# Performance work log

Measured on AMD Instinct MI355X. Metric: run time of the kernel, lower is better.

Reference implementation:

```python
import jax, jax.numpy as jnp
import numpy as np

N_HEADS = 16
HEAD_DIM = 64
ATTN_WINDOW = 128
ROPE_BASE = 10000.0


def _rotate_half(x):
    # (x0, x1) -> (-x1, x0) over interleaved pairs in the last dim
    xr = x.reshape(*x.shape[:-1], -1, 2)
    out = jnp.stack((-xr[..., 1], xr[..., 0]), axis=-1)
    return out.reshape(x.shape)


def _rope_cos_sin(T, rotary_dim, base, dtype):
    inv_freq = 1.0 / (base ** (jnp.arange(0, rotary_dim, 2, dtype=jnp.float32) / rotary_dim))
    t = jnp.arange(T, dtype=jnp.float32)
    freqs = t[:, None] * inv_freq[None, :]            # (T, rotary_dim/2)
    cos = jnp.repeat(jnp.cos(freqs), 2, axis=-1)      # (T, rotary_dim)
    sin = jnp.repeat(jnp.sin(freqs), 2, axis=-1)
    return cos.astype(dtype), sin.astype(dtype)


def _apply_rope(x, cos, sin):
    # x: (B, H, T, Dh); rotary_dim == Dh here (rope_fraction = 1.0)
    c = cos[None, None, :, :]
    s = sin[None, None, :, :]
    return x * c + _rotate_half(x) * s


def setup_inputs() -> dict:
    key = jax.random.key(0)
    ks = jax.random.split(key, 5)
    B, T, C = 2, 2048, 1024
    x = jax.random.normal(ks[0], (B, T, C), dtype=jnp.float32)
    Wqkv = jax.random.normal(ks[1], (C, 3 * C), dtype=jnp.float32) * 0.02
    bqkv = jax.random.normal(ks[2], (3 * C,), dtype=jnp.float32) * 0.02
    Wproj = jax.random.normal(ks[3], (C, C), dtype=jnp.float32) * 0.02
    bproj = jax.random.normal(ks[4], (C,), dtype=jnp.float32) * 0.02
    return {"x": x, "Wqkv": Wqkv, "bqkv": bqkv, "Wproj": Wproj, "bproj": bproj}


def reference(x, Wqkv, bqkv, Wproj, bproj):
    B, T, C = x.shape
    H, Dh = N_HEADS, HEAD_DIM

    qkv = x @ Wqkv + bqkv                              # (B, T, 3C)
    q, k, v = jnp.split(qkv, 3, axis=-1)

    def heads(t):
        return t.reshape(B, T, H, Dh).transpose(0, 2, 1, 3)  # (B, H, T, Dh)
    q, k, v = heads(q), heads(k), heads(v)

    cos, sin = _rope_cos_sin(T, Dh, ROPE_BASE, x.dtype)
    q = _apply_rope(q, cos, sin)
    k = _apply_rope(k, cos, sin)

    # local causal mask: allowed iff 0 <= i - j < attn_window
    idx = jnp.arange(T)
    rel = idx[:, None] - idx[None, :]
    allowed = (rel >= 0) & (rel < ATTN_WINDOW)         # (T, T)

    scale = 1.0 / jnp.sqrt(jnp.asarray(Dh, dtype=x.dtype))
    scores = jnp.einsum("bhqd,bhkd->bhqk", q, k) * scale
    scores = jnp.where(allowed[None, None], scores, jnp.asarray(-jnp.inf, dtype=x.dtype))
    attn = jax.nn.softmax(scores, axis=-1)
    attn_out = jnp.einsum("bhqk,bhkd->bhqd", attn, v)  # (B, H, T, Dh)

    attn_out = attn_out.transpose(0, 2, 1, 3).reshape(B, T, C)
    return attn_out @ Wproj + bproj
```

## Files before the change

### kernel.cpp

```cpp
#include <hip/hip_runtime.h>


using bf16x8 = short  __attribute__((ext_vector_type(8)));
using f32x4  = float __attribute__((ext_vector_type(4)));

__device__ __forceinline__ float bf2f(unsigned short u) {
    return __uint_as_float(((unsigned int)u) << 16);
}
__device__ __forceinline__ unsigned short f2bf(float f) {
    unsigned int u = __float_as_uint(f);
    u += 0x7fffu + ((u >> 16) & 1u);
    return (unsigned short)(u >> 16);
}

__device__ __forceinline__ void gload_lds16(const unsigned short* g,
                                            unsigned short* l) {
    __builtin_amdgcn_global_load_lds(
        (const __attribute__((address_space(1))) unsigned int*)(g),
        (__attribute__((address_space(3))) unsigned int*)(l),
        16, 0, 0);
}

template <int N>
__device__ __forceinline__ void vm_wait() {
    static_assert(N == 0 || N == 2 || N == 3 || N == 4 || N == 6, "add case");
    if constexpr (N == 0)      asm volatile("s_waitcnt vmcnt(0)" ::: "memory");
    else if constexpr (N == 2) asm volatile("s_waitcnt vmcnt(2)" ::: "memory");
    else if constexpr (N == 3) asm volatile("s_waitcnt vmcnt(3)" ::: "memory");
    else if constexpr (N == 4) asm volatile("s_waitcnt vmcnt(4)" ::: "memory");
    else                       asm volatile("s_waitcnt vmcnt(6)" ::: "memory");
}
__device__ __forceinline__ void lgkm_wait0() {
    asm volatile("s_waitcnt lgkmcnt(0)" ::: "memory");
}

__global__ __launch_bounds__(256) void prep_kernel(
        const float* __restrict__ Wqkv, const float* __restrict__ Wproj,
        const float* __restrict__ x,
        unsigned short* __restrict__ WqkvT, unsigned short* __restrict__ WprojT,
        unsigned short* __restrict__ xb, float* __restrict__ tab) {
    __shared__ unsigned short tile[32][33];
    int blk = blockIdx.x;
    int tid = threadIdx.x;
    if (blk < 4096) {
        const float* W; unsigned short* WT; int cols, bx, by;
        if (blk < 3072) { W = Wqkv;  WT = WqkvT;  cols = 3072; bx = blk % 96; by = blk / 96; }
        else            { W = Wproj; WT = WprojT; cols = 1024; bx = (blk - 3072) & 31; by = (blk - 3072) >> 5; }
        int c0 = bx * 32, r0 = by * 32;
        int tx = tid & 31, ty = tid >> 5;
        for (int i = ty; i < 32; i += 8)
            tile[i][tx] = f2bf(W[(size_t)(r0 + i) * cols + c0 + tx]);
        __syncthreads();
        for (int i = ty; i < 32; i += 8)
            WT[(size_t)(c0 + i) * 1024 + r0 + tx] = tile[tx][i];
    } else if (blk < 5120) {
        for (int i = (blk - 4096) * 256 + tid; i < 1048576; i += 262144) {
            float4 v = ((const float4*)x)[i];
            ushort4 o;
            o.x = f2bf(v.x); o.y = f2bf(v.y); o.z = f2bf(v.z); o.w = f2bf(v.w);
            ((ushort4*)xb)[i] = o;
        }
    } else {
        int idx = (blk - 5120) * 256 + tid;
        int t = idx >> 5, i = idx & 31;
        float inv = powf(10000.0f, -(float)i / 32.0f);
        float ang = (float)t * inv;
        tab[idx * 2]     = cosf(ang);
        tab[idx * 2 + 1] = sinf(ang);
    }
}

__global__ __launch_bounds__(256) void gemm1_adirect(
        const unsigned short* __restrict__ A,
        const unsigned short* __restrict__ Bt,
        const float* __restrict__ bias,
        unsigned short* __restrict__ C,
        const float* __restrict__ tab,
        int M, int N, int K) {
    __shared__ unsigned short smem[128 * 128];
    auto Bs = [&](int buf) { return &smem[buf * 128 * 32]; };

    int nwg = gridDim.x * gridDim.y;
    int lid = blockIdx.y * gridDim.x + blockIdx.x;
    int orig = (lid & 7) * (nwg >> 3) + (lid >> 3);
    int bx = orig % gridDim.x, by = orig / gridDim.x;
    int row0 = by * 128, col0 = bx * 128;

    int tid = threadIdx.x;
    int lane = tid & 63, wid = tid >> 6;
    int wr = wid >> 1, wc = wid & 1;
    int fr = lane & 15, kq = lane >> 4;
    int r_in = lane >> 2;
    int scg8 = (((lane & 3) ^ ((lane >> 3) & 3))) * 8;
    int kqs8 = (kq ^ ((fr >> 1) & 3)) * 8;

    f32x4 acc[4][4];
    #pragma unroll
    for (int i = 0; i < 4; ++i)
        #pragma unroll
        for (int j = 0; j < 4; ++j)
            acc[i][j] = (f32x4){0.f, 0.f, 0.f, 0.f};

    auto stageB = [&](int buf, int kt) {
        #pragma unroll
        for (int t = 0; t < 2; ++t) {
            int jb = wid * 2 + t;
            int row = jb * 16 + r_in;
            gload_lds16(Bt + (size_t)(col0 + row) * K + kt + scg8,
                        Bs(buf) + jb * 512);
        }
    };

    const unsigned short* Arow =
        A + (size_t)(row0 + wr * 64 + fr) * K + kq * 8;

    int nt = K >> 5;
    stageB(0, 0);
    for (int t = 0; t < nt; ++t) {
        int kt = t << 5;
        bf16x8 af[4];
        #pragma unroll
        for (int i = 0; i < 4; ++i)
            af[i] = *(const bf16x8*)(Arow + (size_t)(i * 16) * K + kt);
        __builtin_amdgcn_sched_barrier(0);
        if (t + 1 < nt) {
            stageB((t + 1) & 1, kt + 32);
            vm_wait<6>();
        } else {
            vm_wait<4>();
        }
        __builtin_amdgcn_s_barrier();
        bf16x8 bfv[4];
        #pragma unroll
        for (int j = 0; j < 4; ++j)
            bfv[j] = *(const bf16x8*)&Bs(t & 1)[(wc * 64 + j * 16 + fr) * 32 + kqs8];
        #pragma unroll
        for (int i = 0; i < 4; ++i)
            #pragma unroll
            for (int j = 0; j < 4; ++j)
                acc[i][j] = __builtin_amdgcn_mfma_f32_16x16x32_bf16(
                                af[i], bfv[j], acc[i][j], 0, 0, 0);
        if (t + 1 < nt) {
            lgkm_wait0();
            __builtin_amdgcn_s_barrier();
        }
    }

    int rg = kq * 4;
    unsigned short* Ct = smem;
    __syncthreads();
    #pragma unroll
    for (int j = 0; j < 4; ++j) {
        int colL = wc * 64 + j * 16 + fr;
        float bz = bias[col0 + colL];
        #pragma unroll
        for (int i = 0; i < 4; ++i) {
            float v4[4];
            #pragma unroll
            for (int r = 0; r < 4; ++r) v4[r] = acc[i][j][r] + bz;
            if (col0 < 2048) {
                int ii2 = (colL & 63) >> 1;
                bool odd = fr & 1;
                #pragma unroll
                for (int r = 0; r < 4; ++r) {
                    float part = __shfl_xor(v4[r], 1);
                    int trow = (row0 + wr * 64 + i * 16 + rg + r) & 2047;
                    float cc2 = tab[(trow * 32 + ii2) * 2];
                    float ss = tab[(trow * 32 + ii2) * 2 + 1];
                    v4[r] = odd ? fmaf(v4[r], cc2,  part * ss)
                                : fmaf(v4[r], cc2, -part * ss);
                }
            }
            #pragma unroll
            for (int r = 0; r < 4; ++r)
                Ct[(wr * 64 + i * 16 + rg + r) * 128 + colL] = f2bf(v4[r]);
        }
    }
    __syncthreads();
    #pragma unroll
    for (int p = 0; p < 8; ++p) {
        int idx = p * 256 + tid;
        int row = idx >> 4;
        int c8v = (idx & 15) * 8;
        *(bf16x8*)&C[(size_t)(row0 + row) * N + col0 + c8v] =
            *(const bf16x8*)&Ct[row * 128 + c8v];
    }
}

template <int BM, int BN, int WM, int WN, bool OUT_BF16, int DEPTH>
__global__ __launch_bounds__(256) void gemm_lds(
        const unsigned short* __restrict__ A,
        const unsigned short* __restrict__ Bt,
        const float* __restrict__ bias,
        void* __restrict__ Cv,
        int M, int N, int K) {
    constexpr int MI = BM / 16;
    constexpr int NI = BN / 16;
    constexpr int PW = (MI + NI) / 4;
    constexpr int WGN = BN / WN;
    constexpr int MR = WM / 16, NR = WN / 16;

    __shared__ unsigned short smem[DEPTH * (BM + BN) * 32];
    auto As = [&](int buf) { return &smem[buf * (BM + BN) * 32]; };
    auto Bs = [&](int buf) { return &smem[buf * (BM + BN) * 32 + BM * 32]; };

    int nwg = gridDim.x * gridDim.y;
    int lid = blockIdx.y * gridDim.x + blockIdx.x;
    int orig = (lid & 7) * (nwg >> 3) + (lid >> 3);
    int bx = orig % gridDim.x, by = orig / gridDim.x;

    int row0 = by * BM, col0 = bx * BN;
    int tid = threadIdx.x;
    int lane = tid & 63, wid = tid >> 6;
    int wr = wid / WGN, wc = wid % WGN;
    int fr = lane & 15, kq = lane >> 4;
    int r_in = lane >> 2;
    int scg8 = (((lane & 3) ^ ((lane >> 3) & 3))) * 8;
    int kqs8 = (kq ^ ((fr >> 1) & 3)) * 8;

    f32x4 acc[MR][NR];
    #pragma unroll
    for (int i = 0; i < MR; ++i)
        #pragma unroll
        for (int j = 0; j < NR; ++j)
            acc[i][j] = (f32x4){0.f, 0.f, 0.f, 0.f};

    auto stage = [&](int buf, int kt) {
        #pragma unroll
        for (int t = 0; t < PW; ++t) {
            int j = wid * PW + t;
            if (j < MI) {
                int row = j * 16 + r_in;
                gload_lds16(A + (size_t)(row0 + row) * K + kt + scg8,
                            As(buf) + j * 512);
            } else {
                int jb = j - MI;
                int row = jb * 16 + r_in;
                gload_lds16(Bt + (size_t)(col0 + row) * K + kt + scg8,
                            Bs(buf) + jb * 512);
            }
        }
    };
    auto compute = [&](int buf) {
        bf16x8 af[MR], bfv[NR];
        #pragma unroll
        for (int i = 0; i < MR; ++i)
            af[i] = *(const bf16x8*)&As(buf)[(wr * WM + i * 16 + fr) * 32 + kqs8];
        #pragma unroll
        for (int j = 0; j < NR; ++j)
            bfv[j] = *(const bf16x8*)&Bs(buf)[(wc * WN + j * 16 + fr) * 32 + kqs8];
        #pragma unroll
        for (int i = 0; i < MR; ++i)
            #pragma unroll
            for (int j = 0; j < NR; ++j)
                acc[i][j] = __builtin_amdgcn_mfma_f32_16x16x32_bf16(
                                af[i], bfv[j], acc[i][j], 0, 0, 0);
    };

    int nt = K >> 5;
    stage(0, 0);
    if constexpr (DEPTH == 3) stage(1, 32);
    int cc = 0, cs = DEPTH - 1;
    for (int t = 0; t < nt; ++t) {
        int rem = nt - 1 - t;
        if (rem >= DEPTH - 1) {
            stage(cs, (t + DEPTH - 1) << 5);
            vm_wait<(DEPTH - 1) * PW>();
        } else if (rem == 1) {
            vm_wait<PW>();
        } else {
            vm_wait<0>();
        }
        __builtin_amdgcn_s_barrier();
        compute(cc);
        if (t + 1 < nt) {
            lgkm_wait0();
            __builtin_amdgcn_s_barrier();
        }
        cc = (cc + 1 == DEPTH) ? 0 : cc + 1;
        cs = (cs + 1 == DEPTH) ? 0 : cs + 1;
    }

    int rg = kq * 4;
    float* C = (float*)Cv;
    #pragma unroll
    for (int j = 0; j < NR; ++j) {
        int col = col0 + wc * WN + j * 16 + fr;
        float bz = bias[col];
        #pragma unroll
        for (int i = 0; i < MR; ++i) {
            #pragma unroll
            for (int r = 0; r < 4; ++r) {
                int row = row0 + wr * WM + i * 16 + rg + r;
                C[(size_t)row * N + col] = acc[i][j][r] + bz;
            }
        }
    }
}

#define VTS 200
#define PSS 168

__global__ __launch_bounds__(256) void attn_kernel(
        const unsigned short* __restrict__ qkv, unsigned short* __restrict__ aout) {
    __shared__ unsigned short Vt[64 * VTS];
    __shared__ unsigned short Ps[4 * 16 * PSS];

    int bid = blockIdx.x;
    int h  = bid & 15;
    int qt = (bid >> 4) & 31;
    int b  = bid >> 9;
    int Q0 = qt * 64;
    int kbase = Q0 - 127; if (kbase < 0) kbase = 0;
    int nk = Q0 + 64 - kbase;
    int tid = threadIdx.x;

    {
        int r32 = tid & 31;
        int c8  = (tid >> 5) * 8;
        #pragma unroll
        for (int p = 0; p < 7; ++p) {
            int r = p * 32 + r32;
            if (r < VTS) {
                unsigned int wv[4] = {0u, 0u, 0u, 0u};
                if (r < nk) {
                    uint4 v = *(const uint4*)(qkv +
                        (size_t)(b * 2048 + kbase + r) * 3072 + 2048 + h * 64 + c8);
                    wv[0] = v.x; wv[1] = v.y; wv[2] = v.z; wv[3] = v.w;
                }
                #pragma unroll
                for (int j = 0; j < 4; ++j) {
                    Vt[(c8 + 2 * j)     * VTS + r] = (unsigned short)(wv[j] & 0xffffu);
                    Vt[(c8 + 2 * j + 1) * VTS + r] = (unsigned short)(wv[j] >> 16);
                }
            }
        }
    }
    __syncthreads();

    int lane = tid & 63, w = tid >> 6;
    int qw0 = Q0 + w * 16;
    int lo = lane & 15, hi = lane >> 4;

    const unsigned short* qg =
        qkv + (size_t)(b * 2048 + qw0 + lo) * 3072 + h * 64 + hi * 8;
    bf16x8 aq0 = *(const bf16x8*)qg;
    bf16x8 aq1 = *(const bf16x8*)(qg + 32);

    int klo = qw0 - 127; if (klo < kbase) klo = kbase;
    int t0 = (klo - kbase) >> 4;
    int t1 = (qw0 + 15 - kbase) >> 4;
    int ntiles = t1 - t0 + 1;
    if ((ntiles & 1) && t0 > 0) { --t0; ++ntiles; }
    int nks = (ntiles + 1) >> 1;
    int wkb = t0 * 16;

    f32x4 s[10];
    #pragma unroll
    for (int i = 0; i < 10; ++i) s[i] = (f32x4){0.f, 0.f, 0.f, 0.f};
    #pragma unroll
    for (int i = 0; i < 10; ++i) {
        if (i < ntiles) {
            const unsigned short* kg = qkv +
                (size_t)(b * 2048 + kbase + (t0 + i) * 16 + lo) * 3072
                + 1024 + h * 64 + hi * 8;
            bf16x8 bk0 = *(const bf16x8*)kg;
            bf16x8 bk1 = *(const bf16x8*)(kg + 32);
            __builtin_amdgcn_s_setprio(1);
            s[i] = __builtin_amdgcn_mfma_f32_16x16x32_bf16(aq0, bk0, s[i], 0, 0, 0);
            s[i] = __builtin_amdgcn_mfma_f32_16x16x32_bf16(aq1, bk1, s[i], 0, 0, 0);
            __builtin_amdgcn_s_setprio(0);
        }
    }

    const float scale = 0.125f;
    float mx[4] = {-1e30f, -1e30f, -1e30f, -1e30f};
    #pragma unroll
    for (int i = 0; i < 10; ++i) {
        if (i < ntiles) {
            int ka = kbase + (t0 + i) * 16 + lo;
            #pragma unroll
            for (int r = 0; r < 4; ++r) {
                int rel = (qw0 + hi * 4 + r) - ka;
                bool ok = (rel >= 0) && (rel < 128);
                float v = ok ? s[i][r] * scale : -1e30f;
                s[i][r] = v;
                mx[r] = fmaxf(mx[r], v);
            }
        }
    }
    #pragma unroll
    for (int r = 0; r < 4; ++r)
        #pragma unroll
        for (int o = 1; o < 16; o <<= 1)
            mx[r] = fmaxf(mx[r], __shfl_xor(mx[r], o));

    float sum[4] = {0.f, 0.f, 0.f, 0.f};
    #pragma unroll
    for (int i = 0; i < 10; ++i) {
        if (i < ntiles) {
            #pragma unroll
            for (int r = 0; r < 4; ++r) {
                float e = __expf(s[i][r] - mx[r]);
                s[i][r] = e;
                sum[r] += e;
            }
        }
    }
    #pragma unroll
    for (int r = 0; r < 4; ++r) {
        #pragma unroll
        for (int o = 1; o < 16; o <<= 1)
            sum[r] += __shfl_xor(sum[r], o);
        sum[r] = 1.0f / sum[r];
    }

    unsigned short* pw = &Ps[(w * 16) * PSS];
    #pragma unroll
    for (int i = 0; i < 10; ++i) {
        if (i < ntiles) {
            #pragma unroll
            for (int r = 0; r < 4; ++r)
                pw[(hi * 4 + r) * PSS + i * 16 + lo] = f2bf(s[i][r] * sum[r]);
        }
    }
    if (ntiles & 1) {
        int zr = lane >> 2, zc = ntiles * 16 + (lane & 3) * 4;
        *(ushort4*)&pw[zr * PSS + zc] = (ushort4){0, 0, 0, 0};
    }

    f32x4 o[4];
    #pragma unroll
    for (int dt = 0; dt < 4; ++dt) o[dt] = (f32x4){0.f, 0.f, 0.f, 0.f};
    #pragma unroll
    for (int ks = 0; ks < 5; ++ks) {
        if (ks < nks) {
            bf16x8 pa = *(const bf16x8*)&Ps[(w * 16 + lo) * PSS + ks * 32 + hi * 8];
            __builtin_amdgcn_s_setprio(1);
            #pragma unroll
            for (int dt = 0; dt < 4; ++dt) {
                bf16x8 vb = *(const bf16x8*)&Vt[(dt * 16 + lo) * VTS
                                                + wkb + ks * 32 + hi * 8];
                o[dt] = __builtin_amdgcn_mfma_f32_16x16x32_bf16(pa, vb, o[dt], 0, 0, 0);
            }
            __builtin_amdgcn_s_setprio(0);
        }
    }

    #pragma unroll
    for (int dt = 0; dt < 4; ++dt)
        #pragma unroll
        for (int r = 0; r < 4; ++r)
            aout[(size_t)(b * 2048 + qw0 + hi * 4 + r) * 1024
                 + h * 64 + dt * 16 + lo] = f2bf(o[dt][r]);
}

extern "C" void kernel_launch(void* const* d_in, const int* in_sizes, int n_in,
                              void* d_out, int out_size, void* d_ws, size_t ws_size,
                              hipStream_t stream) {
    const float* x     = (const float*)d_in[0];
    const float* Wqkv  = (const float*)d_in[1];
    const float* bqkv  = (const float*)d_in[2];
    const float* Wproj = (const float*)d_in[3];
    const float* bproj = (const float*)d_in[4];
    float* out = (float*)d_out;

    char* ws = (char*)d_ws;
    unsigned short* WqkvT  = (unsigned short*)(ws);
    unsigned short* WprojT = (unsigned short*)(ws + 6291456);
    unsigned short* xb     = (unsigned short*)(ws + 8388608);
    unsigned short* qkv    = (unsigned short*)(ws + 16777216);
    float*          tab    = (float*)        (ws + 41943040);
    unsigned short* attno  = (unsigned short*)(ws + 42467328);

    prep_kernel<<<5376, 256, 0, stream>>>(Wqkv, Wproj, x, WqkvT, WprojT, xb, tab);

    gemm1_adirect<<<dim3(24, 32), 256, 0, stream>>>(
        xb, WqkvT, bqkv, qkv, tab, 4096, 3072, 1024);
    attn_kernel<<<1024, 256, 0, stream>>>(qkv, attno);
    gemm_lds<128, 64, 32, 64, false, 2>
        <<<dim3(16, 32), 256, 0, stream>>>(attno, WprojT, bproj, out, 4096, 1024, 1024);
}
```

Before: 120.0 us.

## Widen weight transpose tiles and restructure GEMM pipelines with register double-buffered A

The prep kernel now transposes 32x128 tiles using float4 loads and ushort4 stores, which cuts the block count and widens memory accesses. The QKV GEMM double-buffers A fragments in registers across two unrolled k-steps, prefetching the next A and B stages before computing the current one. Both GEMMs replace the fine-grained partial vmcnt waits with full vmcnt(0)+lgkmcnt(0) waits and a single barrier per step, issuing the next stage after the barrier. This removes one barrier per iteration but waits on all outstanding loads, which may expose more memory latency.

```diff
diff --git a/kernel.cpp b/kernel.cpp
--- a/kernel.cpp
+++ b/kernel.cpp
@@ -21,14 +21,8 @@
         16, 0, 0);
 }
 
-template <int N>
-__device__ __forceinline__ void vm_wait() {
-    static_assert(N == 0 || N == 2 || N == 3 || N == 4 || N == 6, "add case");
-    if constexpr (N == 0)      asm volatile("s_waitcnt vmcnt(0)" ::: "memory");
-    else if constexpr (N == 2) asm volatile("s_waitcnt vmcnt(2)" ::: "memory");
-    else if constexpr (N == 3) asm volatile("s_waitcnt vmcnt(3)" ::: "memory");
-    else if constexpr (N == 4) asm volatile("s_waitcnt vmcnt(4)" ::: "memory");
-    else                       asm volatile("s_waitcnt vmcnt(6)" ::: "memory");
+__device__ __forceinline__ void vm_wait0() {
+    asm volatile("s_waitcnt vmcnt(0)" ::: "memory");
 }
 __device__ __forceinline__ void lgkm_wait0() {
     asm volatile("s_waitcnt lgkmcnt(0)" ::: "memory");
@@ -39,29 +33,43 @@
         const float* __restrict__ x,
         unsigned short* __restrict__ WqkvT, unsigned short* __restrict__ WprojT,
         unsigned short* __restrict__ xb, float* __restrict__ tab) {
-    __shared__ unsigned short tile[32][33];
+    __shared__ unsigned short tile[32][130];
     int blk = blockIdx.x;
     int tid = threadIdx.x;
-    if (blk < 4096) {
+    if (blk < 1024) {
         const float* W; unsigned short* WT; int cols, bx, by;
-        if (blk < 3072) { W = Wqkv;  WT = WqkvT;  cols = 3072; bx = blk % 96; by = blk / 96; }
-        else            { W = Wproj; WT = WprojT; cols = 1024; bx = (blk - 3072) & 31; by = (blk - 3072) >> 5; }
-        int c0 = bx * 32, r0 = by * 32;
-        int tx = tid & 31, ty = tid >> 5;
-        for (int i = ty; i < 32; i += 8)
-            tile[i][tx] = f2bf(W[(size_t)(r0 + i) * cols + c0 + tx]);
+        if (blk < 768) { W = Wqkv;  WT = WqkvT;  cols = 3072; bx = blk % 24; by = blk / 24; }
+        else { int b2 = blk - 768; W = Wproj; WT = WprojT; cols = 1024; bx = b2 & 7; by = b2 >> 3; }
+        int c0 = bx * 128, r0 = by * 32;
+        #pragma unroll
+        for (int p = 0; p < 4; ++p) {
+            int idx = p * 256 + tid;
+            int ir = idx >> 5, fc = idx & 31;
+            float4 v = *(const float4*)&W[(size_t)(r0 + ir) * cols + c0 + fc * 4];
+            unsigned short* d = &tile[ir][fc * 4];
+            d[0] = f2bf(v.x); d[1] = f2bf(v.y); d[2] = f2bf(v.z); d[3] = f2bf(v.w);
+        }
         __syncthreads();
-        for (int i = ty; i < 32; i += 8)
-            WT[(size_t)(c0 + i) * 1024 + r0 + tx] = tile[tx][i];
-    } else if (blk < 5120) {
-        for (int i = (blk - 4096) * 256 + tid; i < 1048576; i += 262144) {
+        #pragma unroll
+        for (int p = 0; p < 4; ++p) {
+            int idx = p * 256 + tid;
+            int orow = idx >> 3, u4 = idx & 7;
+            ushort4 o;
+            o.x = tile[u4 * 4 + 0][orow];
+            o.y = tile[u4 * 4 + 1][orow];
+            o.z = tile[u4 * 4 + 2][orow];
+            o.w = tile[u4 * 4 + 3][orow];
+            *(ushort4*)&WT[(size_t)(c0 + orow) * 1024 + r0 + u4 * 4] = o;
+        }
+    } else if (blk < 2048) {
+        for (int i = (blk - 1024) * 256 + tid; i < 1048576; i += 262144) {
             float4 v = ((const float4*)x)[i];
             ushort4 o;
             o.x = f2bf(v.x); o.y = f2bf(v.y); o.z = f2bf(v.z); o.w = f2bf(v.w);
             ((ushort4*)xb)[i] = o;
         }
     } else {
-        int idx = (blk - 5120) * 256 + tid;
+        int idx = (blk - 2048) * 256 + tid;
         int t = idx >> 5, i = idx & 31;
         float inv = powf(10000.0f, -(float)i / 32.0f);
         float ang = (float)t * inv;
@@ -70,7 +78,7 @@
     }
 }
 
-__global__ __launch_bounds__(256) void gemm1_adirect(
+__global__ __launch_bounds__(256) void gemm1_areg(
         const unsigned short* __restrict__ A,
         const unsigned short* __restrict__ Bt,
         const float* __restrict__ bias,
@@ -110,39 +118,42 @@
                         Bs(buf) + jb * 512);
         }
     };
-
     const unsigned short* Arow =
         A + (size_t)(row0 + wr * 64 + fr) * K + kq * 8;
-
-    int nt = K >> 5;
-    stageB(0, 0);
-    for (int t = 0; t < nt; ++t) {
-        int kt = t << 5;
-        bf16x8 af[4];
+    auto loadA = [&](bf16x8* dst, int kt) {
         #pragma unroll
         for (int i = 0; i < 4; ++i)
-            af[i] = *(const bf16x8*)(Arow + (size_t)(i * 16) * K + kt);
-        __builtin_amdgcn_sched_barrier(0);
-        if (t + 1 < nt) {
-            stageB((t + 1) & 1, kt + 32);
-            vm_wait<6>();
-        } else {
-            vm_wait<4>();
-        }
-        __builtin_amdgcn_s_barrier();
+            dst[i] = *(const bf16x8*)(Arow + (size_t)(i * 16) * K + kt);
+    };
+    auto computeR = [&](const bf16x8* af, int buf) {
         bf16x8 bfv[4];
         #pragma unroll
         for (int j = 0; j < 4; ++j)
-            bfv[j] = *(const bf16x8*)&Bs(t & 1)[(wc * 64 + j * 16 + fr) * 32 + kqs8];
+            bfv[j] = *(const bf16x8*)&Bs(buf)[(wc * 64 + j * 16 + fr) * 32 + kqs8];
         #pragma unroll
         for (int i = 0; i < 4; ++i)
             #pragma unroll
             for (int j = 0; j < 4; ++j)
                 acc[i][j] = __builtin_amdgcn_mfma_f32_16x16x32_bf16(
                                 af[i], bfv[j], acc[i][j], 0, 0, 0);
+    };
+
+    bf16x8 afA[4], afB[4];
+    int nt = K >> 5;
+    loadA(afA, 0);
+    stageB(0, 0);
+    for (int t = 0; t < nt; t += 2) {
+        lgkm_wait0();
+        vm_wait0();
+        __builtin_amdgcn_s_barrier();
+        if (t + 1 < nt) { loadA(afB, (t + 1) << 5); stageB(1, (t + 1) << 5); }
+        computeR(afA, 0);
         if (t + 1 < nt) {
             lgkm_wait0();
+            vm_wait0();
             __builtin_amdgcn_s_barrier();
+            if (t + 2 < nt) { loadA(afA, (t + 2) << 5); stageB(0, (t + 2) << 5); }
+            computeR(afB, 1);
         }
     }
 
@@ -187,12 +198,12 @@
     }
 }
 
-template <int BM, int BN, int WM, int WN, bool OUT_BF16, int DEPTH>
+template <int BM, int BN, int WM, int WN>
 __global__ __launch_bounds__(256) void gemm_lds(
         const unsigned short* __restrict__ A,
         const unsigned short* __restrict__ Bt,
         const float* __restrict__ bias,
-        void* __restrict__ Cv,
+        float* __restrict__ C,
         int M, int N, int K) {
     constexpr int MI = BM / 16;
     constexpr int NI = BN / 16;
@@ -200,7 +211,7 @@
     constexpr int WGN = BN / WN;
     constexpr int MR = WM / 16, NR = WN / 16;
 
-    __shared__ unsigned short smem[DEPTH * (BM + BN) * 32];
+    __shared__ unsigned short smem[2 * (BM + BN) * 32];
     auto As = [&](int buf) { return &smem[buf * (BM + BN) * 32]; };
     auto Bs = [&](int buf) { return &smem[buf * (BM + BN) * 32 + BM * 32]; };
 
@@ -259,30 +270,16 @@
 
     int nt = K >> 5;
     stage(0, 0);
-    if constexpr (DEPTH == 3) stage(1, 32);
-    int cc = 0, cs = DEPTH - 1;
     for (int t = 0; t < nt; ++t) {
-        int rem = nt - 1 - t;
-        if (rem >= DEPTH - 1) {
-            stage(cs, (t + DEPTH - 1) << 5);
-            vm_wait<(DEPTH - 1) * PW>();
-        } else if (rem == 1) {
-            vm_wait<PW>();
-        } else {
-            vm_wait<0>();
-        }
+        lgkm_wait0();
+        vm_wait0();
         __builtin_amdgcn_s_barrier();
-        compute(cc);
-        if (t + 1 < nt) {
-            lgkm_wait0();
-            __builtin_amdgcn_s_barrier();
-        }
-        cc = (cc + 1 == DEPTH) ? 0 : cc + 1;
-        cs = (cs + 1 == DEPTH) ? 0 : cs + 1;
+        if (t + 1 < nt)
+            stage((t + 1) & 1, (t + 1) << 5);
+        compute(t & 1);
     }
 
     int rg = kq * 4;
-    float* C = (float*)Cv;
     #pragma unroll
     for (int j = 0; j < NR; ++j) {
         int col = col0 + wc * WN + j * 16 + fr;
@@ -473,11 +470,11 @@
     float*          tab    = (float*)        (ws + 41943040);
     unsigned short* attno  = (unsigned short*)(ws + 42467328);
 
-    prep_kernel<<<5376, 256, 0, stream>>>(Wqkv, Wproj, x, WqkvT, WprojT, xb, tab);
-
-    gemm1_adirect<<<dim3(24, 32), 256, 0, stream>>>(
+    prep_kernel<<<2304, 256, 0, stream>>>(Wqkv, Wproj, x, WqkvT, WprojT, xb, tab);
+
+    gemm1_areg<<<dim3(24, 32), 256, 0, stream>>>(
         xb, WqkvT, bqkv, qkv, tab, 4096, 3072, 1024);
     attn_kernel<<<1024, 256, 0, stream>>>(qkv, attno);
-    gemm_lds<128, 64, 32, 64, false, 2>
+    gemm_lds<128, 64, 32, 64>
         <<<dim3(16, 32), 256, 0, stream>>>(attno, WprojT, bproj, out, 4096, 1024, 1024);
 }
```

After: 136.7 us. 1.14x slower.
